# Kernel optimization log

Measured on AMD Instinct MI355X. Metric: run time of the kernel, lower is better.

The kernel has to match this reference:

```python
import jax, jax.numpy as jnp
import numpy as np

B, F, T = 2, 512, 512
D, N, H = 1024, 16, 64   # hidden, heads, head_dim
K = 32                   # time-bias MLP kernal_size
FILT = 4096              # FFN filter size
L = 4                    # num_decoder_blocks
EPS = 1e-6


def _glorot(key, shape, fan_in, fan_out):
    lim = np.sqrt(6.0 / (fan_in + fan_out)).astype(np.float32)
    return jax.random.uniform(key, shape, jnp.float32, -lim, lim)


def setup_inputs() -> dict:
    key = jax.random.key(0)
    ks = jax.random.split(key, 18)
    inp = {
        'decoder_inputs': jax.random.normal(ks[0], (B, F, D), jnp.float32),
        'encoder_outputs': jax.random.normal(ks[1], (B, T, D), jnp.float32),
        'decoder_times_dist': jax.random.uniform(ks[2], (B, F, F), jnp.float32),
        'decoder_encoder_times_dist': jax.random.uniform(ks[3], (B, F, T), jnp.float32),
        'dec_self_attn_bias': jnp.zeros((B, 1, 1, F), jnp.float32),
        'enc_dec_attn_bias': jnp.zeros((B, 1, 1, T), jnp.float32),
        # per-block stacked parameters (leading dim L)
        'Wq': _glorot(ks[4], (L, D, N, H), D, D),
        'Wk': _glorot(ks[5], (L, D, N, H), D, D),
        'Wv': _glorot(ks[6], (L, D, N, H), D, D),
        'Wo': _glorot(ks[7], (L, N, H, D), D, D),
        'Wth': _glorot(ks[8], (L, 1, K), 1, K),
        'bth': jnp.zeros((L, K), jnp.float32),
        'Wto': _glorot(ks[9], (L, K, 1), K, 1),
        'bto': jnp.zeros((L, 1), jnp.float32),
        'Wf1': _glorot(ks[10], (L, D, FILT), D, FILT),
        'bf1': jnp.zeros((L, FILT), jnp.float32),
        'Wf2': _glorot(ks[11], (L, FILT, D), FILT, D),
        'bf2': jnp.zeros((L, D), jnp.float32),
    }
    return inp


def _norm(x):
    # non-trainable LayerNormalization: (x - mean) / (std + eps)
    m = jnp.mean(x, axis=-1, keepdims=True)
    s = jnp.sqrt(jnp.mean((x - m) ** 2, axis=-1, keepdims=True))
    return (x - m) / (s + EPS)


def _attention(x, src, dist, bias, Wq, Wk, Wv, Wo, Wth, bth, Wto, bto):
    q = jnp.einsum('bfd,dnh->bfnh', x, Wq) * (H ** -0.5)
    k = jnp.einsum('btd,dnh->btnh', src, Wk)
    v = jnp.einsum('btd,dnh->btnh', src, Wv)
    # learned time bias: [B,F,T,1] -> relu MLP(K) -> 1 -> [B,F,T]
    hbias = jax.nn.relu(dist[..., None] @ Wth + bth)        # [B,F,T,K]
    qs_bias = (hbias @ Wto + bto)[..., 0]                   # [B,F,T]
    logits = jnp.einsum('btnh,bfnh->bnft', k, q)            # [B,N,F,T]
    logits = logits + bias + qs_bias[:, None]
    w = jax.nn.softmax(logits, axis=-1)
    out = jnp.einsum('bnft,btnh->bfnh', w, v)
    return jnp.einsum('bfnh,nhd->bfd', out, Wo)


def reference(decoder_inputs, encoder_outputs, decoder_times_dist,
              decoder_encoder_times_dist, dec_self_attn_bias, enc_dec_attn_bias,
              Wq, Wk, Wv, Wo, Wth, bth, Wto, bto, Wf1, bf1, Wf2, bf2):
    # decoder_times_dist / dec_self_attn_bias are accepted but unused (as in source call)
    x = decoder_inputs
    for i in range(L):
        # enc-dec attention with pre-norm + residual
        y = _attention(_norm(x), encoder_outputs, decoder_encoder_times_dist,
                       enc_dec_attn_bias, Wq[i], Wk[i], Wv[i], Wo[i],
                       Wth[i], bth[i], Wto[i], bto[i])
        x = x + y
        # FFN with pre-norm + residual
        y = jax.nn.relu(_norm(x) @ Wf1[i] + bf1[i]) @ Wf2[i] + bf2[i]
        x = x + y
    return _norm(x)
```

## Files before the change

### kernel.cpp

```cpp
#include <hip/hip_runtime.h>

typedef unsigned short u16;
typedef __attribute__((ext_vector_type(8))) unsigned short u16x8;
typedef __attribute__((ext_vector_type(4))) unsigned short u16x4;
typedef __attribute__((ext_vector_type(4))) float f32x4;

#define DEVI __device__ __forceinline__

DEVI u16 f2bf(float f){
  unsigned u = __float_as_uint(f);
  u += 0x7FFFu + ((u >> 16) & 1u);
  return (u16)(u >> 16);
}

DEVI void gload16(const void* g, void* l){
  __builtin_amdgcn_global_load_lds((const __attribute__((address_space(1))) void*)g,
                                   (__attribute__((address_space(3))) void*)l, 16, 0, 0);
}

DEVI float wave_sum(float v){
#pragma unroll
  for (int o = 32; o; o >>= 1) v += __shfl_xor(v, o, 64);
  return v;
}

#define MFMA16(a,b,c) __builtin_amdgcn_mfma_f32_16x16x32_bf16((a),(b),(c),0,0,0)

__global__ __launch_bounds__(256) void f32_to_bf16_k(const float* __restrict__ in,
                                                     u16* __restrict__ out, int n4){
  int i = blockIdx.x * 256 + threadIdx.x;
  if (i < n4){
    float4 v = ((const float4*)in)[i];
    u16x4 o = { f2bf(v.x), f2bf(v.y), f2bf(v.z), f2bf(v.w) };
    ((u16x4*)out)[i] = o;
  }
}

__global__ __launch_bounds__(256) void trans_f32_bf16_k(const float* __restrict__ in0,
                                                        u16* __restrict__ out0, int R, int C){
  __shared__ u16 tile[32][33];
  const float* in = in0 + (size_t)blockIdx.z * R * C;
  u16* out = out0 + (size_t)blockIdx.z * R * C;
  const int c0 = blockIdx.x * 32, r0 = blockIdx.y * 32;
  const int tx = threadIdx.x & 31, ty = threadIdx.x >> 5;
#pragma unroll
  for (int k = 0; k < 4; k++)
    tile[ty + k*8][tx] = f2bf(in[(size_t)(r0 + ty + k*8) * C + c0 + tx]);
  __syncthreads();
#pragma unroll
  for (int k = 0; k < 4; k++)
    out[(size_t)(c0 + ty + k*8) * R + r0 + tx] = tile[tx][ty + k*8];
}

__global__ __launch_bounds__(256) void trans4_f32_bf16_k(
    const float* __restrict__ Wq, const float* __restrict__ Wk,
    const float* __restrict__ Wv, const float* __restrict__ Wo,
    u16* __restrict__ Wqt, u16* __restrict__ Wkt,
    u16* __restrict__ Wvt, u16* __restrict__ Wot){
  __shared__ u16 tile[32][33];
  const int z = blockIdx.z, sel = z >> 2, l = z & 3;
  const float* in = (sel == 0 ? Wq : sel == 1 ? Wk : sel == 2 ? Wv : Wo) + (size_t)l * 1048576;
  u16* out = (sel == 0 ? Wqt : sel == 1 ? Wkt : sel == 2 ? Wvt : Wot) + (size_t)l * 1048576;
  const int c0 = blockIdx.x * 32, r0 = blockIdx.y * 32;
  const int tx = threadIdx.x & 31, ty = threadIdx.x >> 5;
#pragma unroll
  for (int k = 0; k < 4; k++)
    tile[ty + k*8][tx] = f2bf(in[(size_t)(r0 + ty + k*8) * 1024 + c0 + tx]);
  __syncthreads();
#pragma unroll
  for (int k = 0; k < 4; k++)
    out[(size_t)(c0 + ty + k*8) * 1024 + r0 + tx] = tile[tx][ty + k*8];
}

__global__ __launch_bounds__(256) void vtrans_k(const u16* __restrict__ V0, u16* __restrict__ Vt0){
  __shared__ u16 tile[32][33];
  const int t0 = blockIdx.x * 32;
  const int h0 = blockIdx.y * 32;
  const int z = blockIdx.z, l = z >> 5, bn = z & 31;
  const int b = bn >> 4, n = bn & 15;
  const u16* V = V0 + (size_t)l * 1048576;
  u16* Vt = Vt0 + (size_t)l * 1048576;
  const int tx = threadIdx.x & 31, ty = threadIdx.x >> 5;
#pragma unroll
  for (int k = 0; k < 4; k++)
    tile[ty + k*8][tx] = V[(size_t)(b*512 + t0 + ty + k*8) * 1024 + n*64 + h0 + tx];
  __syncthreads();
#pragma unroll
  for (int k = 0; k < 4; k++)
    Vt[(size_t)((b*16 + n)*64 + h0 + ty + k*8) * 512 + t0 + tx] = tile[tx][ty + k*8];
}

__global__ __launch_bounds__(256) void layernorm_k(const float* __restrict__ in, u16* __restrict__ outp){
  const int row = blockIdx.x;
  const int tid = threadIdx.x;
  const float4 v = ((const float4*)(in + (size_t)row * 1024))[tid];
  __shared__ float sb[8];
  const int wid = tid >> 6, lane = tid & 63;
  float s = wave_sum(v.x + v.y + v.z + v.w);
  if (lane == 0) sb[wid] = s;
  __syncthreads();
  const float mean = (sb[0] + sb[1] + sb[2] + sb[3]) * (1.0f / 1024.0f);
  const float dx = v.x - mean, dy = v.y - mean, dz = v.z - mean, dw = v.w - mean;
  float q = wave_sum(dx*dx + dy*dy + dz*dz + dw*dw);
  if (lane == 0) sb[4 + wid] = q;
  __syncthreads();
  const float sd = sqrtf((sb[4] + sb[5] + sb[6] + sb[7]) * (1.0f / 1024.0f));
  const float inv = 1.0f / (sd + 1e-6f);
  u16x4 o = { f2bf(dx*inv), f2bf(dy*inv), f2bf(dz*inv), f2bf(dw*inv) };
  ((u16x4*)outp)[(size_t)row * 256 + tid] = o;
}

__global__ __launch_bounds__(256) void qsbias_k(const float* __restrict__ dist,
    const float* __restrict__ Wth0, const float* __restrict__ bth0,
    const float* __restrict__ Wto0, const float* __restrict__ bto0,
    float* __restrict__ qs0){
  const int ly = blockIdx.y;
  const float* Wth = Wth0 + ly*32;
  const float* bth = bth0 + ly*32;
  const float* Wto = Wto0 + ly*32;
  float* qs = qs0 + (size_t)ly * 524288;
  const int idx = blockIdx.x * 256 + threadIdx.x;
  float4 s4 = ((const float4*)dist)[idx];
  float sv[4] = { s4.x, s4.y, s4.z, s4.w };
  float r[4];
  const float b0 = bto0[ly];
#pragma unroll
  for (int c = 0; c < 4; c++) r[c] = b0;
#pragma unroll
  for (int k = 0; k < 32; k++){
    const float wk = Wth[k], bk = bth[k], ok = Wto[k];
#pragma unroll
    for (int c = 0; c < 4; c++){
      float h = fmaxf(sv[c] * wk + bk, 0.0f);
      r[c] += h * ok;
    }
  }
  ((float4*)qs)[idx] = make_float4(r[0], r[1], r[2], r[3]);
}

template<int MODE, int BN>
DEVI void gemm128_core(const u16* A, int lda, const u16* Bt, int ldb,
                       int Klen, int Nd, void* Cout,
                       const float* bias, float scale,
                       u16* Als, u16* Bls, int row0, int col0){
  constexpr int WN = BN / 2, FN = BN / 32;
  constexpr int BSZ = BN * 64;
  const int tid = threadIdx.x;
  const int wid = tid >> 6, lane = tid & 63;
  const int wm = wid >> 1, wn = wid & 1;
  const int lrow = lane & 15, g = lane >> 4, e7 = lane & 7;
  f32x4 acc[4][FN] = {};

  const int scol = ((lane & 7) ^ ((lane >> 3) & 7)) * 8;
  const u16* Ag = A + (size_t)(row0 + wid*8 + (lane >> 3)) * lda + scol;
  const u16* Bg = Bt + (size_t)(col0 + wid*8 + (lane >> 3)) * ldb + scol;
  const int dst0 = wid * 512;

  const int nt = Klen >> 6;

#define STAGE128(buf, k0)                                                     \
  {                                                                           \
    _Pragma("unroll")                                                         \
    for (int q = 0; q < 4; q++)                                               \
      gload16(Ag + (size_t)q*32*lda + (k0), Als + (buf)*8192 + dst0 + q*2048);\
    _Pragma("unroll")                                                         \
    for (int q = 0; q < BN/32; q++)                                           \
      gload16(Bg + (size_t)q*32*ldb + (k0), Bls + (buf)*BSZ + dst0 + q*2048); \
  }

  STAGE128(0, 0);
  __syncthreads();

  for (int t = 0; t < nt; t++){
    const int cur = t & 1;
    if (t + 1 < nt) STAGE128(cur ^ 1, (t + 1) << 6);
    const u16* Ab = Als + cur * 8192;
    const u16* Bb = Bls + cur * BSZ;
#pragma unroll
    for (int ks = 0; ks < 2; ks++){
      const int sl = (((ks << 2) + g) ^ e7) << 3;
      u16x8 av[4], bv[FN];
#pragma unroll
      for (int mi = 0; mi < 4; mi++)
        av[mi] = *(const u16x8*)(Ab + (wm*64 + mi*16 + lrow) * 64 + sl);
#pragma unroll
      for (int ni = 0; ni < FN; ni++)
        bv[ni] = *(const u16x8*)(Bb + (wn*WN + ni*16 + lrow) * 64 + sl);
#pragma unroll
      for (int mi = 0; mi < 4; mi++)
#pragma unroll
        for (int ni = 0; ni < FN; ni++)
          acc[mi][ni] = MFMA16(av[mi], bv[ni], acc[mi][ni]);
    }
    __syncthreads();
  }
#undef STAGE128

#pragma unroll
  for (int mi = 0; mi < 4; mi++){
#pragma unroll
    for (int ni = 0; ni < FN; ni++){
      const int col = col0 + wn*WN + ni*16 + lrow;
#pragma unroll
      for (int j = 0; j < 4; j++){
        const int row = row0 + wm*64 + mi*16 + g*4 + j;
        float v = acc[mi][ni][j];
        if (MODE == 3) v = fmaxf(v + bias[col], 0.0f);
        if (MODE == 0 || MODE == 3)
          ((u16*)Cout)[(size_t)row * Nd + col] = f2bf(v);
        else
          ((float*)Cout)[(size_t)row * Nd + col] = v;
      }
    }
  }
}

template<int MODE>
__global__ __launch_bounds__(256) void gemm128_k(const u16* __restrict__ A, int lda,
    const u16* __restrict__ Bt, int ldb, int Klen, int Nd, void* __restrict__ Cout,
    const float* __restrict__ bias, float scale){
  __shared__ __align__(16) u16 Als[2 * 8192];
  __shared__ __align__(16) u16 Bls[2 * 4096];
  gemm128_core<MODE, 64>(A, lda, Bt, ldb, Klen, Nd, Cout, bias, scale,
                         Als, Bls, blockIdx.y * 128, blockIdx.x * 64);
}

__global__ __launch_bounds__(256) void gemmKV_k(const u16* __restrict__ encb,
    const u16* __restrict__ Wkt, const u16* __restrict__ Wvt,
    u16* __restrict__ Kb, u16* __restrict__ Vb){
  __shared__ __align__(16) u16 Als[2 * 8192];
  __shared__ __align__(16) u16 Bls[2 * 4096];
  const int z = blockIdx.z, l = z >> 1;
  const u16* Bt = ((z & 1) ? Wvt : Wkt) + (size_t)l * 1048576;
  u16* out = ((z & 1) ? Vb : Kb) + (size_t)l * 1048576;
  gemm128_core<0, 64>(encb, 1024, Bt, 1024, 1024, 1024, out, nullptr, 1.0f,
                      Als, Bls, blockIdx.y * 128, blockIdx.x * 64);
}

__global__ __launch_bounds__(256) void gemm_splitk_k(const u16* __restrict__ A, int lda,
    const u16* __restrict__ Bt, int ldb, int Klen, float* __restrict__ part){
  __shared__ __align__(16) u16 Als[2 * 8192];
  __shared__ __align__(16) u16 Bls[2 * 4096];
  const int z = blockIdx.z;
  gemm128_core<5, 64>(A + (size_t)z * Klen, lda, Bt + (size_t)z * Klen, ldb, Klen, 1024,
                      part + (size_t)z * 1048576, nullptr, 1.0f,
                      Als, Bls, blockIdx.y * 128, blockIdx.x * 64);
}

template<int BIAS, int LAST>
__global__ __launch_bounds__(256) void reduce_ln_k(const float* __restrict__ part,
    const float* __restrict__ bias, float* __restrict__ x, u16* __restrict__ xn,
    float* __restrict__ dout){
  const int row = blockIdx.x, tid = threadIdx.x;
  const size_t idx = (size_t)row * 256 + tid;
  float4 v = ((const float4*)x)[idx];
  float4 p0 = ((const float4*)part)[idx];
  float4 p1 = ((const float4*)(part + 1048576))[idx];
  float4 p2 = ((const float4*)(part + 2097152))[idx];
  float4 p3 = ((const float4*)(part + 3145728))[idx];
  v.x += p0.x + p1.x + p2.x + p3.x;
  v.y += p0.y + p1.y + p2.y + p3.y;
  v.z += p0.z + p1.z + p2.z + p3.z;
  v.w += p0.w + p1.w + p2.w + p3.w;
  if (BIAS){
    const float4 b = *(const float4*)(bias + tid * 4);
    v.x += b.x; v.y += b.y; v.z += b.z; v.w += b.w;
  }
  if (!LAST) ((float4*)x)[idx] = v;

  __shared__ float sb[8];
  const int wid = tid >> 6, lane = tid & 63;
  float s = wave_sum(v.x + v.y + v.z + v.w);
  if (lane == 0) sb[wid] = s;
  __syncthreads();
  const float mean = (sb[0] + sb[1] + sb[2] + sb[3]) * (1.0f / 1024.0f);
  const float dx = v.x - mean, dy = v.y - mean, dz = v.z - mean, dw = v.w - mean;
  float q = wave_sum(dx*dx + dy*dy + dz*dz + dw*dw);
  if (lane == 0) sb[4 + wid] = q;
  __syncthreads();
  const float sd = sqrtf((sb[4] + sb[5] + sb[6] + sb[7]) * (1.0f / 1024.0f));
  const float inv = 1.0f / (sd + 1e-6f);
  if (LAST){
    ((float4*)dout)[idx] = make_float4(dx*inv, dy*inv, dz*inv, dw*inv);
  } else {
    u16x4 o = { f2bf(dx*inv), f2bf(dy*inv), f2bf(dz*inv), f2bf(dw*inv) };
    ((u16x4*)xn)[idx] = o;
  }
}

__global__ __launch_bounds__(256, 1) void attn_k(const float* __restrict__ partQ,
    const u16* __restrict__ Kb, const u16* __restrict__ Vt,
    const float* __restrict__ qs, const float* __restrict__ abias,
    u16* __restrict__ aout){
  const int n = blockIdx.x, f0 = blockIdx.y * 64, b = blockIdx.z;
  const int w = threadIdx.x >> 6, lane = threadIdx.x & 63;
  const int l15 = lane & 15, g = lane >> 4, e7 = lane & 7;
  const int fw = f0 + w * 16;
  __shared__ __align__(16) u16 Pl[4][16 * 512];
  u16* pw = &Pl[w][0];

  u16x8 qf0, qf1;
  {
    const float* pq = partQ + ((size_t)b*512 + fw + l15) * 1024 + n*64 + g*8;
    float q0[8] = {0,0,0,0,0,0,0,0}, q1[8] = {0,0,0,0,0,0,0,0};
#pragma unroll
    for (int z = 0; z < 4; z++){
      const float* p = pq + (size_t)z * 1048576;
#pragma unroll
      for (int e = 0; e < 8; e++){ q0[e] += p[e]; q1[e] += p[e + 32]; }
    }
#pragma unroll
    for (int e = 0; e < 8; e++){
      qf0[e] = f2bf(q0[e] * 0.125f);
      qf1[e] = f2bf(q1[e] * 0.125f);
    }
  }

  f32x4 acc[32];
  const u16* kp = Kb + ((size_t)b*512 + l15) * 1024 + n*64 + g*8;
#pragma unroll
  for (int tf = 0; tf < 32; tf++){
    u16x8 k0 = *(const u16x8*)(kp + (size_t)tf*16*1024);
    u16x8 k1 = *(const u16x8*)(kp + (size_t)tf*16*1024 + 32);
    f32x4 z = {0.f, 0.f, 0.f, 0.f};
    z = MFMA16(k0, qf0, z);
    acc[tf] = MFMA16(k1, qf1, z);
  }

  const float* qsp = qs + ((size_t)b*512 + fw + l15) * 512 + g*4;
  const float* abp = abias + (size_t)b*512 + g*4;
  float m = -3.0e38f;
#pragma unroll
  for (int tf = 0; tf < 32; tf++){
    float4 qv = *(const float4*)(qsp + tf*16);
    float4 av = *(const float4*)(abp + tf*16);
    acc[tf][0] += qv.x + av.x;
    acc[tf][1] += qv.y + av.y;
    acc[tf][2] += qv.z + av.z;
    acc[tf][3] += qv.w + av.w;
    m = fmaxf(m, fmaxf(fmaxf(acc[tf][0], acc[tf][1]), fmaxf(acc[tf][2], acc[tf][3])));
  }
  m = fmaxf(m, __shfl_xor(m, 16, 64));
  m = fmaxf(m, __shfl_xor(m, 32, 64));

  float s = 0.f;
#pragma unroll
  for (int tf = 0; tf < 32; tf++){
#pragma unroll
    for (int j = 0; j < 4; j++){
      float e = __expf(acc[tf][j] - m);
      acc[tf][j] = e; s += e;
    }
  }
  s += __shfl_xor(s, 16, 64);
  s += __shfl_xor(s, 32, 64);
  const float inv = 1.0f / s;
  float invj[4];
#pragma unroll
  for (int j = 0; j < 4; j++) invj[j] = __shfl(inv, g*4 + j, 64);

#pragma unroll
  for (int tf = 0; tf < 32; tf++){
    const int chunk = tf*2 + (g >> 1);
    const int boff = (l15 << 10) + ((chunk ^ e7) << 4) + ((g & 1) << 3);
    u16x4 pk = { f2bf(acc[tf][0]), f2bf(acc[tf][1]), f2bf(acc[tf][2]), f2bf(acc[tf][3]) };
    *(u16x4*)((char*)pw + boff) = pk;
  }

  f32x4 oacc[4] = {};
  const u16* vp = Vt + ((size_t)(b*16 + n)*64 + l15) * 512 + g*8;
  for (int kk = 0; kk < 16; kk++){
    u16x8 pa = *(const u16x8*)((char*)pw + (l15 << 10) + ((((kk << 2) + g) ^ e7) << 4));
#pragma unroll
    for (int nf = 0; nf < 4; nf++){
      u16x8 vb = *(const u16x8*)(vp + (size_t)nf*16*512 + kk*32);
      oacc[nf] = MFMA16(pa, vb, oacc[nf]);
    }
  }

  u16* op = aout + ((size_t)b*512 + fw + g*4) * 1024 + n*64 + l15;
#pragma unroll
  for (int nf = 0; nf < 4; nf++)
#pragma unroll
    for (int j = 0; j < 4; j++)
      op[(size_t)j*1024 + nf*16] = f2bf(oacc[nf][j] * invj[j]);
}

extern "C" void kernel_launch(void* const* d_in, const int* in_sizes, int n_in,
                              void* d_out, int out_size, void* d_ws, size_t ws_size,
                              hipStream_t stream){
  const float* dec_in   = (const float*)d_in[0];
  const float* enc      = (const float*)d_in[1];
  const float* dist     = (const float*)d_in[3];
  const float* abias    = (const float*)d_in[5];
  const float* Wq  = (const float*)d_in[6];
  const float* Wk  = (const float*)d_in[7];
  const float* Wv  = (const float*)d_in[8];
  const float* Wo  = (const float*)d_in[9];
  const float* Wth = (const float*)d_in[10];
  const float* bth = (const float*)d_in[11];
  const float* Wto = (const float*)d_in[12];
  const float* bto = (const float*)d_in[13];
  const float* Wf1 = (const float*)d_in[14];
  const float* bf1 = (const float*)d_in[15];
  const float* Wf2 = (const float*)d_in[16];
  const float* bf2 = (const float*)d_in[17];
  float* dout = (float*)d_out;

  char* wp = (char*)d_ws;
  auto alloc = [&](size_t n) -> char* {
    char* p = wp; wp += (n + 255) & ~(size_t)255; return p;
  };
  float* x     = (float*)alloc((size_t)1048576 * 4);
  u16*  xn     = (u16*)alloc((size_t)1048576 * 2);
  u16*  encb   = (u16*)alloc((size_t)1048576 * 2);
  u16*  Wqt    = (u16*)alloc((size_t)4194304 * 2);
  u16*  Wkt    = (u16*)alloc((size_t)4194304 * 2);
  u16*  Wvt    = (u16*)alloc((size_t)4194304 * 2);
  u16*  Wot    = (u16*)alloc((size_t)4194304 * 2);
  u16*  Wf1t   = (u16*)alloc((size_t)16777216 * 2);
  u16*  Wf2t   = (u16*)alloc((size_t)16777216 * 2);
  u16*  Kb     = (u16*)alloc((size_t)4194304 * 2);
  u16*  Vb     = (u16*)alloc((size_t)4194304 * 2);
  u16*  Vt     = (u16*)alloc((size_t)4194304 * 2);
  float* qs    = (float*)alloc((size_t)2097152 * 4);
  u16*  aout   = (u16*)alloc((size_t)1048576 * 2);
  u16*  ffh    = (u16*)alloc((size_t)4194304 * 2);
  float* part  = (float*)alloc((size_t)4194304 * 4);

  hipMemcpyAsync(x, dec_in, (size_t)1048576 * 4, hipMemcpyDeviceToDevice, stream);
  f32_to_bf16_k<<<1024, 256, 0, stream>>>(enc, encb, 262144);

  trans4_f32_bf16_k<<<dim3(32, 32, 16), 256, 0, stream>>>(Wq, Wk, Wv, Wo, Wqt, Wkt, Wvt, Wot);
  trans_f32_bf16_k<<<dim3(128, 32, 4), 256, 0, stream>>>(Wf1, Wf1t, 1024, 4096);
  trans_f32_bf16_k<<<dim3(32, 128, 4), 256, 0, stream>>>(Wf2, Wf2t, 4096, 1024);

  qsbias_k<<<dim3(512, 4), 256, 0, stream>>>(dist, Wth, bth, Wto, bto, qs);

  gemmKV_k<<<dim3(16, 8, 8), 256, 0, stream>>>(encb, Wkt, Wvt, Kb, Vb);
  vtrans_k<<<dim3(16, 2, 128), 256, 0, stream>>>(Vb, Vt);

  layernorm_k<<<1024, 256, 0, stream>>>(x, xn);

  for (int i = 0; i < 4; i++){
    const size_t wo = (size_t)i * 1048576;

    gemm_splitk_k<<<dim3(16, 8, 4), 256, 0, stream>>>(xn, 1024, Wqt + wo, 1024, 256, part);

    attn_k<<<dim3(16, 8, 2), 256, 0, stream>>>(part, Kb + wo, Vt + wo,
                                               qs + (size_t)i * 524288, abias, aout);

    gemm_splitk_k<<<dim3(16, 8, 4), 256, 0, stream>>>(aout, 1024, Wot + wo, 1024, 256, part);
    reduce_ln_k<0, 0><<<1024, 256, 0, stream>>>(part, nullptr, x, xn, nullptr);

    gemm128_k<3><<<dim3(64, 8), 256, 0, stream>>>(xn, 1024, Wf1t + (size_t)i*4194304, 1024,
                                                  1024, 4096, ffh, bf1 + (size_t)i*4096, 1.0f);
    gemm_splitk_k<<<dim3(16, 8, 4), 256, 0, stream>>>(ffh, 4096, Wf2t + (size_t)i*4194304, 4096,
                                                      1024, part);
    if (i < 3)
      reduce_ln_k<1, 0><<<1024, 256, 0, stream>>>(part, bf2 + (size_t)i*1024, x, xn, nullptr);
    else
      reduce_ln_k<1, 1><<<1024, 256, 0, stream>>>(part, bf2 + (size_t)i*1024, x, nullptr, dout);
  }
}
```

Baseline: 489.1 us.

## Fuse Q projection into attention, emit V transposed from GEMM, merge prep kernels

The attention kernel now computes its own Q tile (64 rows x one head) from the normalized activations and Wq using an LDS-staged MFMA loop, which removes the split-K Q GEMM launch and its fp32 partial round-trip. The V projection is computed as Wv^T·enc^T with a new epilogue mode that writes directly in the transposed per-head layout, which eliminates the separate V transpose kernel and buffer. All weight and encoder conversions are merged into one large prep kernel. The cost is redundant Q computation work inside attention (each block streams a 1024-deep K loop) and fewer launches overall.

```diff
diff --git a/kernel.cpp b/kernel.cpp
--- a/kernel.cpp
+++ b/kernel.cpp
@@ -26,22 +26,39 @@
 
 #define MFMA16(a,b,c) __builtin_amdgcn_mfma_f32_16x16x32_bf16((a),(b),(c),0,0,0)
 
-__global__ __launch_bounds__(256) void f32_to_bf16_k(const float* __restrict__ in,
-                                                     u16* __restrict__ out, int n4){
-  int i = blockIdx.x * 256 + threadIdx.x;
-  if (i < n4){
-    float4 v = ((const float4*)in)[i];
+__global__ __launch_bounds__(256) void prep_k(
+    const float* __restrict__ Wq, const float* __restrict__ Wk,
+    const float* __restrict__ Wv, const float* __restrict__ Wo,
+    const float* __restrict__ Wf1, const float* __restrict__ Wf2,
+    const float* __restrict__ enc,
+    u16* __restrict__ Wqt, u16* __restrict__ Wkt,
+    u16* __restrict__ Wvt, u16* __restrict__ Wot,
+    u16* __restrict__ Wf1t, u16* __restrict__ Wf2t,
+    u16* __restrict__ encb){
+  __shared__ u16 tile[32][33];
+  const int t = blockIdx.x;
+  if (t >= 49152){
+    const int i = (t - 49152) * 256 + threadIdx.x;
+    float4 v = ((const float4*)enc)[i];
     u16x4 o = { f2bf(v.x), f2bf(v.y), f2bf(v.z), f2bf(v.w) };
-    ((u16x4*)out)[i] = o;
-  }
-}
-
-__global__ __launch_bounds__(256) void trans_f32_bf16_k(const float* __restrict__ in0,
-                                                        u16* __restrict__ out0, int R, int C){
-  __shared__ u16 tile[32][33];
-  const float* in = in0 + (size_t)blockIdx.z * R * C;
-  u16* out = out0 + (size_t)blockIdx.z * R * C;
-  const int c0 = blockIdx.x * 32, r0 = blockIdx.y * 32;
+    ((u16x4*)encb)[i] = o;
+    return;
+  }
+  const float* in; u16* out; int C, R, r0, c0;
+  if (t < 16384){
+    const int mat = t >> 10, ti = t & 1023, sel = mat >> 2, l = mat & 3;
+    in  = (sel == 0 ? Wq : sel == 1 ? Wk : sel == 2 ? Wv : Wo) + (size_t)l * 1048576;
+    out = (sel == 0 ? Wqt : sel == 1 ? Wkt : sel == 2 ? Wvt : Wot) + (size_t)l * 1048576;
+    R = 1024; C = 1024; r0 = (ti >> 5) * 32; c0 = (ti & 31) * 32;
+  } else if (t < 32768){
+    const int t2 = t - 16384, mat = t2 >> 12, ti = t2 & 4095;
+    in = Wf1 + (size_t)mat * 4194304; out = Wf1t + (size_t)mat * 4194304;
+    R = 1024; C = 4096; r0 = (ti >> 7) * 32; c0 = (ti & 127) * 32;
+  } else {
+    const int t2 = t - 32768, mat = t2 >> 12, ti = t2 & 4095;
+    in = Wf2 + (size_t)mat * 4194304; out = Wf2t + (size_t)mat * 4194304;
+    R = 4096; C = 1024; r0 = (ti >> 5) * 32; c0 = (ti & 31) * 32;
+  }
   const int tx = threadIdx.x & 31, ty = threadIdx.x >> 5;
 #pragma unroll
   for (int k = 0; k < 4; k++)
@@ -50,44 +67,6 @@
 #pragma unroll
   for (int k = 0; k < 4; k++)
     out[(size_t)(c0 + ty + k*8) * R + r0 + tx] = tile[tx][ty + k*8];
-}
-
-__global__ __launch_bounds__(256) void trans4_f32_bf16_k(
-    const float* __restrict__ Wq, const float* __restrict__ Wk,
-    const float* __restrict__ Wv, const float* __restrict__ Wo,
-    u16* __restrict__ Wqt, u16* __restrict__ Wkt,
-    u16* __restrict__ Wvt, u16* __restrict__ Wot){
-  __shared__ u16 tile[32][33];
-  const int z = blockIdx.z, sel = z >> 2, l = z & 3;
-  const float* in = (sel == 0 ? Wq : sel == 1 ? Wk : sel == 2 ? Wv : Wo) + (size_t)l * 1048576;
-  u16* out = (sel == 0 ? Wqt : sel == 1 ? Wkt : sel == 2 ? Wvt : Wot) + (size_t)l * 1048576;
-  const int c0 = blockIdx.x * 32, r0 = blockIdx.y * 32;
-  const int tx = threadIdx.x & 31, ty = threadIdx.x >> 5;
-#pragma unroll
-  for (int k = 0; k < 4; k++)
-    tile[ty + k*8][tx] = f2bf(in[(size_t)(r0 + ty + k*8) * 1024 + c0 + tx]);
-  __syncthreads();
-#pragma unroll
-  for (int k = 0; k < 4; k++)
-    out[(size_t)(c0 + ty + k*8) * 1024 + r0 + tx] = tile[tx][ty + k*8];
-}
-
-__global__ __launch_bounds__(256) void vtrans_k(const u16* __restrict__ V0, u16* __restrict__ Vt0){
-  __shared__ u16 tile[32][33];
-  const int t0 = blockIdx.x * 32;
-  const int h0 = blockIdx.y * 32;
-  const int z = blockIdx.z, l = z >> 5, bn = z & 31;
-  const int b = bn >> 4, n = bn & 15;
-  const u16* V = V0 + (size_t)l * 1048576;
-  u16* Vt = Vt0 + (size_t)l * 1048576;
-  const int tx = threadIdx.x & 31, ty = threadIdx.x >> 5;
-#pragma unroll
-  for (int k = 0; k < 4; k++)
-    tile[ty + k*8][tx] = V[(size_t)(b*512 + t0 + ty + k*8) * 1024 + n*64 + h0 + tx];
-  __syncthreads();
-#pragma unroll
-  for (int k = 0; k < 4; k++)
-    Vt[(size_t)((b*16 + n)*64 + h0 + ty + k*8) * 512 + t0 + tx] = tile[tx][ty + k*8];
 }
 
 __global__ __launch_bounds__(256) void layernorm_k(const float* __restrict__ in, u16* __restrict__ outp){
@@ -208,6 +187,9 @@
         if (MODE == 3) v = fmaxf(v + bias[col], 0.0f);
         if (MODE == 0 || MODE == 3)
           ((u16*)Cout)[(size_t)row * Nd + col] = f2bf(v);
+        else if (MODE == 6)
+          ((u16*)Cout)[(size_t)((col >> 9)*16 + (row >> 6)) * 32768
+                       + (row & 63) * 512 + (col & 511)] = f2bf(v);
         else
           ((float*)Cout)[(size_t)row * Nd + col] = v;
       }
@@ -227,14 +209,18 @@
 
 __global__ __launch_bounds__(256) void gemmKV_k(const u16* __restrict__ encb,
     const u16* __restrict__ Wkt, const u16* __restrict__ Wvt,
-    u16* __restrict__ Kb, u16* __restrict__ Vb){
+    u16* __restrict__ Kb, u16* __restrict__ Vt){
   __shared__ __align__(16) u16 Als[2 * 8192];
   __shared__ __align__(16) u16 Bls[2 * 4096];
   const int z = blockIdx.z, l = z >> 1;
-  const u16* Bt = ((z & 1) ? Wvt : Wkt) + (size_t)l * 1048576;
-  u16* out = ((z & 1) ? Vb : Kb) + (size_t)l * 1048576;
-  gemm128_core<0, 64>(encb, 1024, Bt, 1024, 1024, 1024, out, nullptr, 1.0f,
-                      Als, Bls, blockIdx.y * 128, blockIdx.x * 64);
+  if ((z & 1) == 0)
+    gemm128_core<0, 64>(encb, 1024, Wkt + (size_t)l*1048576, 1024, 1024, 1024,
+                        Kb + (size_t)l*1048576, nullptr, 1.0f,
+                        Als, Bls, blockIdx.y * 128, blockIdx.x * 64);
+  else
+    gemm128_core<6, 64>(Wvt + (size_t)l*1048576, 1024, encb, 1024, 1024, 1024,
+                        Vt + (size_t)l*1048576, nullptr, 1.0f,
+                        Als, Bls, blockIdx.y * 128, blockIdx.x * 64);
 }
 
 __global__ __launch_bounds__(256) void gemm_splitk_k(const u16* __restrict__ A, int lda,
@@ -288,7 +274,8 @@
   }
 }
 
-__global__ __launch_bounds__(256, 1) void attn_k(const float* __restrict__ partQ,
+__global__ __launch_bounds__(256, 1) void attn_k(const u16* __restrict__ xn,
+    const u16* __restrict__ Wqt,
     const u16* __restrict__ Kb, const u16* __restrict__ Vt,
     const float* __restrict__ qs, const float* __restrict__ abias,
     u16* __restrict__ aout){
@@ -301,19 +288,66 @@
 
   u16x8 qf0, qf1;
   {
-    const float* pq = partQ + ((size_t)b*512 + fw + l15) * 1024 + n*64 + g*8;
-    float q0[8] = {0,0,0,0,0,0,0,0}, q1[8] = {0,0,0,0,0,0,0,0};
-#pragma unroll
-    for (int z = 0; z < 4; z++){
-      const float* p = pq + (size_t)z * 1048576;
-#pragma unroll
-      for (int e = 0; e < 8; e++){ q0[e] += p[e]; q1[e] += p[e + 32]; }
-    }
-#pragma unroll
-    for (int e = 0; e < 8; e++){
-      qf0[e] = f2bf(q0[e] * 0.125f);
-      qf1[e] = f2bf(q1[e] * 0.125f);
-    }
+    u16* Als = &Pl[0][0];
+    u16* Bls = &Pl[1][0];
+    const int wm = w >> 1, wn = w & 1;
+    f32x4 qac[2][2] = {};
+    const int scol = ((lane & 7) ^ ((lane >> 3) & 7)) * 8;
+    const u16* Ag = xn + (size_t)(b*512 + f0 + w*8 + (lane >> 3)) * 1024 + scol;
+    const u16* Bg = Wqt + (size_t)(n*64 + w*8 + (lane >> 3)) * 1024 + scol;
+    const int dq = w * 512;
+
+#define STAGEQ(buf, k0)                                         \
+    gload16(Ag + (k0),            Als + (buf)*4096 + dq);       \
+    gload16(Ag + 32*1024 + (k0),  Als + (buf)*4096 + dq + 2048);\
+    gload16(Bg + (k0),            Bls + (buf)*4096 + dq);       \
+    gload16(Bg + 32*1024 + (k0),  Bls + (buf)*4096 + dq + 2048);
+
+    STAGEQ(0, 0);
+    __syncthreads();
+    for (int t = 0; t < 16; t++){
+      const int cur = t & 1;
+      if (t < 15){ STAGEQ(cur ^ 1, (t + 1) << 6); }
+      const u16* Ab = Als + cur * 4096;
+      const u16* Bb = Bls + cur * 4096;
+#pragma unroll
+      for (int ks = 0; ks < 2; ks++){
+        const int sl = (((ks << 2) + g) ^ e7) << 3;
+        u16x8 av[2], bv[2];
+#pragma unroll
+        for (int mi = 0; mi < 2; mi++)
+          av[mi] = *(const u16x8*)(Ab + (wm*32 + mi*16 + l15) * 64 + sl);
+#pragma unroll
+        for (int ni = 0; ni < 2; ni++)
+          bv[ni] = *(const u16x8*)(Bb + (wn*32 + ni*16 + l15) * 64 + sl);
+#pragma unroll
+        for (int mi = 0; mi < 2; mi++)
+#pragma unroll
+          for (int ni = 0; ni < 2; ni++)
+            qac[mi][ni] = MFMA16(av[mi], bv[ni], qac[mi][ni]);
+      }
+      __syncthreads();
+    }
+#undef STAGEQ
+
+    u16* Qt = &Pl[2][0];
+#pragma unroll
+    for (int mi = 0; mi < 2; mi++)
+#pragma unroll
+      for (int ni = 0; ni < 2; ni++)
+#pragma unroll
+        for (int j = 0; j < 4; j++){
+          const int r = wm*32 + mi*16 + g*4 + j;
+          const int c = wn*32 + ni*16 + l15;
+          const int byte = r*128 + (((c >> 3) ^ (r & 7)) << 4) + (c & 7)*2;
+          *(u16*)((char*)Qt + byte) = f2bf(qac[mi][ni][j] * 0.125f);
+        }
+    __syncthreads();
+    const int r = w*16 + l15;
+    const char* qrow = (char*)Qt + r*128;
+    qf0 = *(const u16x8*)(qrow + ((g ^ (r & 7)) << 4));
+    qf1 = *(const u16x8*)(qrow + (((4 + g) ^ (r & 7)) << 4));
+    __syncthreads();
   }
 
   f32x4 acc[32];
@@ -421,7 +455,6 @@
   u16*  Wf1t   = (u16*)alloc((size_t)16777216 * 2);
   u16*  Wf2t   = (u16*)alloc((size_t)16777216 * 2);
   u16*  Kb     = (u16*)alloc((size_t)4194304 * 2);
-  u16*  Vb     = (u16*)alloc((size_t)4194304 * 2);
   u16*  Vt     = (u16*)alloc((size_t)4194304 * 2);
   float* qs    = (float*)alloc((size_t)2097152 * 4);
   u16*  aout   = (u16*)alloc((size_t)1048576 * 2);
@@ -429,25 +462,16 @@
   float* part  = (float*)alloc((size_t)4194304 * 4);
 
   hipMemcpyAsync(x, dec_in, (size_t)1048576 * 4, hipMemcpyDeviceToDevice, stream);
-  f32_to_bf16_k<<<1024, 256, 0, stream>>>(enc, encb, 262144);
-
-  trans4_f32_bf16_k<<<dim3(32, 32, 16), 256, 0, stream>>>(Wq, Wk, Wv, Wo, Wqt, Wkt, Wvt, Wot);
-  trans_f32_bf16_k<<<dim3(128, 32, 4), 256, 0, stream>>>(Wf1, Wf1t, 1024, 4096);
-  trans_f32_bf16_k<<<dim3(32, 128, 4), 256, 0, stream>>>(Wf2, Wf2t, 4096, 1024);
-
+  prep_k<<<50176, 256, 0, stream>>>(Wq, Wk, Wv, Wo, Wf1, Wf2, enc,
+                                    Wqt, Wkt, Wvt, Wot, Wf1t, Wf2t, encb);
   qsbias_k<<<dim3(512, 4), 256, 0, stream>>>(dist, Wth, bth, Wto, bto, qs);
-
-  gemmKV_k<<<dim3(16, 8, 8), 256, 0, stream>>>(encb, Wkt, Wvt, Kb, Vb);
-  vtrans_k<<<dim3(16, 2, 128), 256, 0, stream>>>(Vb, Vt);
-
+  gemmKV_k<<<dim3(16, 8, 8), 256, 0, stream>>>(encb, Wkt, Wvt, Kb, Vt);
   layernorm_k<<<1024, 256, 0, stream>>>(x, xn);
 
   for (int i = 0; i < 4; i++){
     const size_t wo = (size_t)i * 1048576;
 
-    gemm_splitk_k<<<dim3(16, 8, 4), 256, 0, stream>>>(xn, 1024, Wqt + wo, 1024, 256, part);
-
-    attn_k<<<dim3(16, 8, 2), 256, 0, stream>>>(part, Kb + wo, Vt + wo,
+    attn_k<<<dim3(16, 8, 2), 256, 0, stream>>>(xn, Wqt + wo, Kb + wo, Vt + wo,
                                                qs + (size_t)i * 524288, abias, aout);
 
     gemm_splitk_k<<<dim3(16, 8, 4), 256, 0, stream>>>(aout, 1024, Wot + wo, 1024, 256, part);
```

Result: faster. 454.5 us (-7.1%).
